# Optimization experiments

Hardware: AMD Instinct MI355X
Metric: run time of the kernel (lower is better)

Reference implementation:

```python
import jax, jax.numpy as jnp
import numpy as np
import math

DIM = 1024
HEADS = 16
B, N = 2, 2048

POLY = jnp.array([-0.037, 0.481, -2.3, 4.917, -1.791], dtype=jnp.float32)


def adaptive_temperature_softmax(logits):
    # logits: [b, h, n, n]
    original_probs = jax.nn.softmax(logits, axis=-1)
    entropy = jnp.sum(-original_probs * jnp.log(original_probs + 1e-9), axis=-1, keepdims=True)
    e2 = entropy * entropy
    poly_result = POLY[0] * e2 * e2 + POLY[1] * e2 * entropy + POLY[2] * e2 + POLY[3] * entropy + POLY[4]
    beta = jnp.where(entropy > 0.5, jnp.maximum(poly_result, 1.0), 1.0)
    return jax.nn.softmax(logits * beta, axis=-1)


def setup_inputs() -> dict:
    key = jax.random.key(0)
    ks = jax.random.split(key, 5)
    s = 1.0 / math.sqrt(DIM)
    return {
        "x": jax.random.normal(ks[0], (B, N, DIM), dtype=jnp.float32),
        "Wq": jax.random.normal(ks[1], (DIM, DIM), dtype=jnp.float32) * s,
        "Wk": jax.random.normal(ks[2], (DIM, DIM), dtype=jnp.float32) * s,
        "Wv": jax.random.normal(ks[3], (DIM, DIM), dtype=jnp.float32) * s,
        "Wo": jax.random.normal(ks[4], (DIM, DIM), dtype=jnp.float32) * s,
        "bo": jnp.zeros((DIM,), dtype=jnp.float32),
    }


def reference(x, Wq, Wk, Wv, Wo, bo):
    b, n, d = x.shape
    h = HEADS
    hd = d // h
    # torch nn.Linear: y = x @ W.T (+ bias)
    def proj(W):
        t = x @ W.T  # [b, n, d]
        return t.reshape(b, n, h, hd).transpose(0, 2, 1, 3)  # [b, h, n, hd]
    q, k, v = proj(Wq), proj(Wk), proj(Wv)
    sim = jnp.einsum('bhid,bhjd->bhij', q, k) / math.sqrt(hd)
    neg = -jnp.finfo(sim.dtype).max
    causal = jnp.triu(jnp.ones((n, n), dtype=bool), k=1)  # True above diagonal
    sim = jnp.where(causal, neg, sim)
    attn = adaptive_temperature_softmax(sim)
    out = jnp.einsum('bhij,bhjd->bhid', attn, v)
    out = out.transpose(0, 2, 1, 3).reshape(b, n, d)
    return out @ Wo.T + bo
```

## Files before the change

### kernel.cpp

```cpp
#include <hip/hip_runtime.h>
#include <math.h>

#define B_   2
#define N_   2048
#define D_   1024
#define H_   16
#define HD_  64
#define BH_  32
#define M_   4096

typedef __bf16 bf16x8 __attribute__((ext_vector_type(8)));
typedef float  f32x4  __attribute__((ext_vector_type(4)));

#define AS1_ __attribute__((address_space(1)))
#define AS3_ __attribute__((address_space(3)))
#define GLDS16(g, l) __builtin_amdgcn_global_load_lds( \
    (const AS1_ void*)(g), (AS3_ void*)(l), 16, 0, 0)

__device__ inline unsigned short f2b(float f) {
    unsigned u = __float_as_uint(f);
    u += 0x7FFFu + ((u >> 16) & 1u);
    return (unsigned short)(u >> 16);
}
__device__ inline unsigned short f2b_fast(float f) {
    return (unsigned short)((__float_as_uint(f) + 0x8000u) >> 16);
}

__global__ __launch_bounds__(256)
void cvt_all(const float* __restrict__ x,  const float* __restrict__ wq,
             const float* __restrict__ wk, const float* __restrict__ wv,
             const float* __restrict__ wo, ushort* __restrict__ dst)
{
    int i = blockIdx.x * 256 + threadIdx.x;
    if (i >= 2097152) return;
    int fi = i * 4;
    const float* s; int off;
    if (fi < 4194304) { s = x; off = fi; }
    else {
        int r = fi - 4194304;
        int wsel = r >> 20;
        off = r & 1048575;
        s = (wsel == 0) ? wq : (wsel == 1) ? wk : (wsel == 2) ? wv : wo;
    }
    float4 f = *(const float4*)(s + off);
    ushort4 o;
    o.x = f2b(f.x); o.y = f2b(f.y); o.z = f2b(f.z); o.w = f2b(f.w);
    *(ushort4*)(dst + fi) = o;
}

__global__ __launch_bounds__(256)
void gemm_qkv(const ushort* __restrict__ A,
              const ushort* __restrict__ W0, const ushort* __restrict__ W1,
              const ushort* __restrict__ W2,
              ushort* __restrict__ O0, ushort* __restrict__ O1,
              ushort* __restrict__ O2)
{
    const int z = blockIdx.z;
    const ushort* W = (z == 0) ? W0 : (z == 1) ? W1 : W2;

    __shared__ alignas(16) ushort As[128][32];
    __shared__ alignas(16) ushort Bs[128][32];

    const int t = threadIdx.x;
    const int lane = t & 63, w = t >> 6;
    const int quad = lane >> 4, l15 = lane & 15;
    const int wm = (w >> 1) * 64, wn = (w & 1) * 64;
    const int tileM = blockIdx.x * 128, tileN = blockIdx.y * 128;

    const int srow = lane >> 2, scol = (lane & 3) * 8;
    const ushort* GA = A + (size_t)(tileM + w * 16 + srow) * D_ + scol;
    const ushort* GB = W + (size_t)(tileN + w * 16 + srow) * D_ + scol;

    f32x4 acc[4][4];
#pragma unroll
    for (int mt = 0; mt < 4; ++mt)
#pragma unroll
        for (int nt = 0; nt < 4; ++nt) acc[mt][nt] = (f32x4){0.f, 0.f, 0.f, 0.f};

    for (int k0 = 0; k0 < D_; k0 += 32) {
        __syncthreads();
        GLDS16(GA + k0,            &As[w * 16][0]);
        GLDS16(GA + 64 * D_ + k0,  &As[64 + w * 16][0]);
        GLDS16(GB + k0,            &Bs[w * 16][0]);
        GLDS16(GB + 64 * D_ + k0,  &Bs[64 + w * 16][0]);
        __syncthreads();

        bf16x8 af[4], bf[4];
#pragma unroll
        for (int mt = 0; mt < 4; ++mt) af[mt] = *(const bf16x8*)&As[wm + mt * 16 + l15][quad * 8];
#pragma unroll
        for (int nt = 0; nt < 4; ++nt) bf[nt] = *(const bf16x8*)&Bs[wn + nt * 16 + l15][quad * 8];
#pragma unroll
        for (int mt = 0; mt < 4; ++mt)
#pragma unroll
            for (int nt = 0; nt < 4; ++nt)
                acc[mt][nt] = __builtin_amdgcn_mfma_f32_16x16x32_bf16(af[mt], bf[nt], acc[mt][nt], 0, 0, 0);
    }

    ushort* O = (z == 0) ? O0 : (z == 1) ? O1 : O2;
    const float scl = (z == 0) ? 0.18033688f : 1.0f;
#pragma unroll
    for (int mt = 0; mt < 4; ++mt)
#pragma unroll
        for (int nt = 0; nt < 4; ++nt) {
            if (z == 2) {
                int rg0 = tileM + wm + mt * 16 + quad * 4;
                int cgc = tileN + wn + nt * 16 + l15;
                int b = rg0 >> 11, n0 = rg0 & (N_ - 1);
                int h = cgc >> 6, dd = cgc & 63;
                ushort4 o4;
                o4.x = f2b(acc[mt][nt][0]); o4.y = f2b(acc[mt][nt][1]);
                o4.z = f2b(acc[mt][nt][2]); o4.w = f2b(acc[mt][nt][3]);
                *(ushort4*)&O[((size_t)((b * H_ + h) * HD_ + dd)) * N_ + n0] = o4;
            } else {
#pragma unroll
                for (int r = 0; r < 4; ++r) {
                    int rg = tileM + wm + mt * 16 + quad * 4 + r;
                    int cgc = tileN + wn + nt * 16 + l15;
                    int b = rg >> 11, n = rg & (N_ - 1);
                    int h = cgc >> 6, dd = cgc & 63;
                    O[(((size_t)(b * H_ + h)) * N_ + n) * HD_ + dd] = f2b(acc[mt][nt][r] * scl);
                }
            }
        }
}

__global__ __launch_bounds__(256)
void gemm_fin(const ushort* __restrict__ A, const ushort* __restrict__ W,
              const float* __restrict__ bias, float* __restrict__ Of)
{
    __shared__ alignas(16) ushort As[128][32];
    __shared__ alignas(16) ushort Bs[64][32];

    const int t = threadIdx.x;
    const int lane = t & 63, w = t >> 6;
    const int quad = lane >> 4, l15 = lane & 15;
    const int wm = (w >> 1) * 64, wn = (w & 1) * 32;
    const int tileM = blockIdx.x * 128, tileN = blockIdx.y * 64;

    const int srow = lane >> 2, scol = (lane & 3) * 8;
    const ushort* GA = A + (size_t)(tileM + w * 16 + srow) * D_ + scol;
    const ushort* GB = W + (size_t)(tileN + w * 16 + srow) * D_ + scol;

    f32x4 acc[4][2];
#pragma unroll
    for (int mt = 0; mt < 4; ++mt)
#pragma unroll
        for (int nt = 0; nt < 2; ++nt) acc[mt][nt] = (f32x4){0.f, 0.f, 0.f, 0.f};

    for (int k0 = 0; k0 < D_; k0 += 32) {
        __syncthreads();
        GLDS16(GA + k0,           &As[w * 16][0]);
        GLDS16(GA + 64 * D_ + k0, &As[64 + w * 16][0]);
        GLDS16(GB + k0,           &Bs[w * 16][0]);
        __syncthreads();

        bf16x8 af[4], bf[2];
#pragma unroll
        for (int mt = 0; mt < 4; ++mt) af[mt] = *(const bf16x8*)&As[wm + mt * 16 + l15][quad * 8];
#pragma unroll
        for (int nt = 0; nt < 2; ++nt) bf[nt] = *(const bf16x8*)&Bs[wn + nt * 16 + l15][quad * 8];
#pragma unroll
        for (int mt = 0; mt < 4; ++mt)
#pragma unroll
            for (int nt = 0; nt < 2; ++nt)
                acc[mt][nt] = __builtin_amdgcn_mfma_f32_16x16x32_bf16(af[mt], bf[nt], acc[mt][nt], 0, 0, 0);
    }

#pragma unroll
    for (int mt = 0; mt < 4; ++mt)
#pragma unroll
        for (int nt = 0; nt < 2; ++nt)
#pragma unroll
            for (int r = 0; r < 4; ++r) {
                int rg = tileM + wm + mt * 16 + quad * 4 + r;
                int cgc = tileN + wn + nt * 16 + l15;
                Of[(size_t)rg * D_ + cgc] = acc[mt][nt][r] + bias[cgc];
            }
}

__global__ __launch_bounds__(256)
void attn_mfma(const ushort* __restrict__ Q, const ushort* __restrict__ K,
               const ushort* __restrict__ VT, ushort* __restrict__ AO)
{
    const int bid = blockIdx.x;
    const int qt = 31 - (bid >> 5);
    const int bh = bid & 31;
    const size_t kvbase = (size_t)bh * N_ * HD_;

    __shared__ alignas(16) ushort Ks[128][72];
    __shared__ alignas(16) ushort Vs[64][136];
    __shared__ alignas(16) ushort Ps[4][4][296];

    const int t = threadIdx.x;
    const int lane = t & 63, w = t >> 6;
    const int quad = lane >> 4, l15 = lane & 15;
    const float SH2 = 11.5416913f;
    const float LN2 = 0.69314718f;

    const int skey = t >> 3;
    const int skc  = (t & 7) * 8;
    const ushort* KS = K + kvbase + (size_t)skey * HD_ + skc;
    const int vhd = t >> 4;
    const int vkc = (t & 15) * 8;
    const ushort* VS = VT + kvbase + (size_t)vhd * N_ + vkc;

    const int qrow = w * 16 + quad * 4;
    const int qglob = qt * 64 + qrow;
    const int b = bh >> 4, h = bh & 15;
    const int nCh = (qt + 2) >> 1;

    bf16x8 aq0, aq1;
    {
        const size_t qr = kvbase + (size_t)(qt * 64 + w * 16 + l15) * HD_;
        aq0 = *(const bf16x8*)&Q[qr + quad * 8];
        aq1 = *(const bf16x8*)&Q[qr + 32 + quad * 8];
    }

    float ez[4] = {0.f, 0.f, 0.f, 0.f};
    float sz[4] = {0.f, 0.f, 0.f, 0.f};

    uint4 k0 = *(const uint4*)KS;
    uint4 k1 = *(const uint4*)(KS + 32 * HD_);
    uint4 k2 = *(const uint4*)(KS + 64 * HD_);
    uint4 k3 = *(const uint4*)(KS + 96 * HD_);
    for (int c = 0; c < nCh; ++c) {
        __syncthreads();
        *(uint4*)&Ks[skey][skc]      = k0;
        *(uint4*)&Ks[32 + skey][skc] = k1;
        *(uint4*)&Ks[64 + skey][skc] = k2;
        *(uint4*)&Ks[96 + skey][skc] = k3;
        __syncthreads();
        if (c + 1 < nCh) {
            const ushort* nb = KS + (size_t)(c + 1) * (128 * HD_);
            k0 = *(const uint4*)nb;
            k1 = *(const uint4*)(nb + 32 * HD_);
            k2 = *(const uint4*)(nb + 64 * HD_);
            k3 = *(const uint4*)(nb + 96 * HD_);
        }
        if (c + 1 < nCh) {
#pragma unroll
            for (int nt = 0; nt < 8; ++nt) {
                f32x4 sv = (f32x4){-SH2, -SH2, -SH2, -SH2};
                sv = __builtin_amdgcn_mfma_f32_16x16x32_bf16(aq0, *(const bf16x8*)&Ks[nt * 16 + l15][quad * 8], sv, 0, 0, 0);
                sv = __builtin_amdgcn_mfma_f32_16x16x32_bf16(aq1, *(const bf16x8*)&Ks[nt * 16 + l15][32 + quad * 8], sv, 0, 0, 0);
#pragma unroll
                for (int r = 0; r < 4; ++r) {
                    float sh = sv[r];
                    float e = __builtin_amdgcn_exp2f(sh);
                    ez[r] += e;
                    sz[r] = fmaf(e, sh, sz[r]);
                }
            }
        } else {
            const int tiles = (((qt + 1) * 64) - c * 128) >> 4;
            const int kb0 = c * 128;
            for (int nt = 0; nt < tiles; ++nt) {
                f32x4 sv = (f32x4){-SH2, -SH2, -SH2, -SH2};
                sv = __builtin_amdgcn_mfma_f32_16x16x32_bf16(aq0, *(const bf16x8*)&Ks[nt * 16 + l15][quad * 8], sv, 0, 0, 0);
                sv = __builtin_amdgcn_mfma_f32_16x16x32_bf16(aq1, *(const bf16x8*)&Ks[nt * 16 + l15][32 + quad * 8], sv, 0, 0, 0);
                const int kcol = kb0 + nt * 16 + l15;
#pragma unroll
                for (int r = 0; r < 4; ++r) {
                    float sh = sv[r];
                    float e = (kcol <= qglob + r) ? __builtin_amdgcn_exp2f(sh) : 0.f;
                    ez[r] += e;
                    sz[r] = fmaf(e, sh, sz[r]);
                }
            }
        }
    }
#pragma unroll
    for (int r = 0; r < 4; ++r) {
#pragma unroll
        for (int off = 1; off < 16; off <<= 1) {
            ez[r] += __shfl_xor(ez[r], off);
            sz[r] += __shfl_xor(sz[r], off);
        }
    }

    float bl[4];
#pragma unroll
    for (int r = 0; r < 4; ++r) {
        float Z = ez[r];
        float Hh = LN2 * (__builtin_amdgcn_logf(Z) - sz[r] / Z);
        float bb = 1.f;
        if (Hh > 0.5f) {
            float e2 = Hh * Hh;
            float pp = -0.037f * e2 * e2 + 0.481f * e2 * Hh - 2.3f * e2 + 4.917f * Hh - 1.791f;
            bb = fmaxf(pp, 1.f);
        }
        bl[r] = bb;
    }

    f32x4 ov[4];
#pragma unroll
    for (int nt = 0; nt < 4; ++nt) ov[nt] = (f32x4){0.f, 0.f, 0.f, 0.f};
    float zp[4] = {0.f, 0.f, 0.f, 0.f};

    k0 = *(const uint4*)KS;
    k1 = *(const uint4*)(KS + 32 * HD_);
    k2 = *(const uint4*)(KS + 64 * HD_);
    k3 = *(const uint4*)(KS + 96 * HD_);
    uint4 v0 = *(const uint4*)VS;
    uint4 v1 = *(const uint4*)(VS + 16 * N_);
    uint4 v2 = *(const uint4*)(VS + 32 * N_);
    uint4 v3 = *(const uint4*)(VS + 48 * N_);
    for (int c = 0; c < nCh; ++c) {
        __syncthreads();
        *(uint4*)&Ks[skey][skc]      = k0;
        *(uint4*)&Ks[32 + skey][skc] = k1;
        *(uint4*)&Ks[64 + skey][skc] = k2;
        *(uint4*)&Ks[96 + skey][skc] = k3;
        *(uint4*)&Vs[vhd][vkc]       = v0;
        *(uint4*)&Vs[16 + vhd][vkc]  = v1;
        *(uint4*)&Vs[32 + vhd][vkc]  = v2;
        *(uint4*)&Vs[48 + vhd][vkc]  = v3;
        __syncthreads();
        if (c + 1 < nCh) {
            const ushort* nk = KS + (size_t)(c + 1) * (128 * HD_);
            k0 = *(const uint4*)nk;
            k1 = *(const uint4*)(nk + 32 * HD_);
            k2 = *(const uint4*)(nk + 64 * HD_);
            k3 = *(const uint4*)(nk + 96 * HD_);
            const ushort* nv = VS + (c + 1) * 128;
            v0 = *(const uint4*)nv;
            v1 = *(const uint4*)(nv + 16 * N_);
            v2 = *(const uint4*)(nv + 32 * N_);
            v3 = *(const uint4*)(nv + 48 * N_);
        }
        const int halves = min(2, (qt + 1) - c * 2);
        for (int hh = 0; hh < halves; ++hh) {
            const bool diag = (c * 2 + hh == qt);

            float wv[4][4];
#pragma unroll
            for (int nt = 0; nt < 4; ++nt) {
                f32x4 sv = (f32x4){-SH2, -SH2, -SH2, -SH2};
                sv = __builtin_amdgcn_mfma_f32_16x16x32_bf16(aq0, *(const bf16x8*)&Ks[hh * 64 + nt * 16 + l15][quad * 8], sv, 0, 0, 0);
                sv = __builtin_amdgcn_mfma_f32_16x16x32_bf16(aq1, *(const bf16x8*)&Ks[hh * 64 + nt * 16 + l15][32 + quad * 8], sv, 0, 0, 0);
                const int kcol = nt * 16 + l15;
#pragma unroll
                for (int r = 0; r < 4; ++r) {
                    float e = __builtin_amdgcn_exp2f(bl[r] * sv[r]);
                    wv[nt][r] = (!diag || (kcol <= qrow + r)) ? e : 0.f;
                }
            }
#pragma unroll
            for (int nt = 0; nt < 4; ++nt)
#pragma unroll
                for (int r = 0; r < 4; ++r)
                    Ps[w][quad][r * 72 + nt * 16 + l15] = f2b_fast(wv[nt][r]);
#pragma unroll
            for (int r = 0; r < 4; ++r)
                zp[r] += (wv[0][r] + wv[1][r]) + (wv[2][r] + wv[3][r]);

            bf16x8 pa0 = *(const bf16x8*)&Ps[w][l15 >> 2][(l15 & 3) * 72 + quad * 8];
            bf16x8 pa1 = *(const bf16x8*)&Ps[w][l15 >> 2][(l15 & 3) * 72 + 32 + quad * 8];
#pragma unroll
            for (int nt = 0; nt < 4; ++nt) {
                ov[nt] = __builtin_amdgcn_mfma_f32_16x16x32_bf16(pa0, *(const bf16x8*)&Vs[nt * 16 + l15][hh * 64 + quad * 8], ov[nt], 0, 0, 0);
                ov[nt] = __builtin_amdgcn_mfma_f32_16x16x32_bf16(pa1, *(const bf16x8*)&Vs[nt * 16 + l15][hh * 64 + 32 + quad * 8], ov[nt], 0, 0, 0);
            }
        }
    }
#pragma unroll
    for (int r = 0; r < 4; ++r)
#pragma unroll
        for (int off = 1; off < 16; off <<= 1) zp[r] += __shfl_xor(zp[r], off);

#pragma unroll
    for (int r = 0; r < 4; ++r) {
        int qg = qt * 64 + w * 16 + quad * 4 + r;
        float inv = 1.f / zp[r];
        size_t rowoff = ((size_t)(b * N_ + qg)) * D_ + h * HD_;
#pragma unroll
        for (int nt = 0; nt < 4; ++nt)
            AO[rowoff + nt * 16 + l15] = f2b(ov[nt][r] * inv);
    }
}

extern "C" void kernel_launch(void* const* d_in, const int* in_sizes, int n_in,
                              void* d_out, int out_size, void* d_ws, size_t ws_size,
                              hipStream_t stream)
{
    const float* x  = (const float*)d_in[0];
    const float* Wq = (const float*)d_in[1];
    const float* Wk = (const float*)d_in[2];
    const float* Wv = (const float*)d_in[3];
    const float* Wo = (const float*)d_in[4];
    const float* bo = (const float*)d_in[5];
    float* out = (float*)d_out;

    ushort* ws  = (ushort*)d_ws;
    ushort* xb  = ws;
    ushort* wqb = ws + 4194304;
    ushort* wkb = ws + 5242880;
    ushort* wvb = ws + 6291456;
    ushort* wob = ws + 7340032;
    ushort* Qb  = ws + 8388608;
    ushort* Kb  = ws + 12582912;
    ushort* Vtb = ws + 16777216;
    ushort* aob = ws + 20971520;

    cvt_all<<<8192, 256, 0, stream>>>(x, Wq, Wk, Wv, Wo, xb);

    gemm_qkv<<<dim3(32, 8, 3), 256, 0, stream>>>(
        xb, wqb, wkb, wvb, Qb, Kb, Vtb);

    attn_mfma<<<dim3(1024), 256, 0, stream>>>(Qb, Kb, Vtb, aob);

    gemm_fin<<<dim3(32, 16), 256, 0, stream>>>(aob, wob, bo, out);
}
```

Before: 207.7 us.

## Double-buffer LDS tiles in QKV and output projection GEMMs

Both projection GEMMs now use two shared-memory buffers. The next K-slice is issued with global_load_lds while MFMAs run on the current slice, and only one barrier is used per iteration instead of two. The aim is to hide global load latency behind compute, at the cost of doubled LDS use per block, which could lower occupancy. The sync before reuse relies on the barrier also waiting for the async LDS loads to land.

After: 202.7 us. -2.4%, faster.

```diff
diff --git a/kernel.cpp b/kernel.cpp
--- a/kernel.cpp
+++ b/kernel.cpp
@@ -58,8 +58,8 @@
     const int z = blockIdx.z;
     const ushort* W = (z == 0) ? W0 : (z == 1) ? W1 : W2;
 
-    __shared__ alignas(16) ushort As[128][32];
-    __shared__ alignas(16) ushort Bs[128][32];
+    __shared__ alignas(16) ushort As[2][128][32];
+    __shared__ alignas(16) ushort Bs[2][128][32];
 
     const int t = threadIdx.x;
     const int lane = t & 63, w = t >> 6;
@@ -67,9 +67,8 @@
     const int wm = (w >> 1) * 64, wn = (w & 1) * 64;
     const int tileM = blockIdx.x * 128, tileN = blockIdx.y * 128;
 
-    const int srow = lane >> 2, scol = (lane & 3) * 8;
-    const ushort* GA = A + (size_t)(tileM + w * 16 + srow) * D_ + scol;
-    const ushort* GB = W + (size_t)(tileN + w * 16 + srow) * D_ + scol;
+    const ushort* GA = A + (size_t)(tileM + w * 16 + (lane >> 2)) * D_ + (lane & 3) * 8;
+    const ushort* GB = W + (size_t)(tileN + w * 16 + (lane >> 2)) * D_ + (lane & 3) * 8;
 
     f32x4 acc[4][4];
 #pragma unroll
@@ -77,24 +76,35 @@
 #pragma unroll
         for (int nt = 0; nt < 4; ++nt) acc[mt][nt] = (f32x4){0.f, 0.f, 0.f, 0.f};
 
+    GLDS16(GA,            &As[0][w * 16][0]);
+    GLDS16(GA + 64 * D_,  &As[0][64 + w * 16][0]);
+    GLDS16(GB,            &Bs[0][w * 16][0]);
+    GLDS16(GB + 64 * D_,  &Bs[0][64 + w * 16][0]);
+    __syncthreads();
+
+    int cur = 0;
     for (int k0 = 0; k0 < D_; k0 += 32) {
-        __syncthreads();
-        GLDS16(GA + k0,            &As[w * 16][0]);
-        GLDS16(GA + 64 * D_ + k0,  &As[64 + w * 16][0]);
-        GLDS16(GB + k0,            &Bs[w * 16][0]);
-        GLDS16(GB + 64 * D_ + k0,  &Bs[64 + w * 16][0]);
-        __syncthreads();
+        const int nxt = cur ^ 1;
+        if (k0 + 32 < D_) {
+            GLDS16(GA + k0 + 32,           &As[nxt][w * 16][0]);
+            GLDS16(GA + 64 * D_ + k0 + 32, &As[nxt][64 + w * 16][0]);
+            GLDS16(GB + k0 + 32,           &Bs[nxt][w * 16][0]);
+            GLDS16(GB + 64 * D_ + k0 + 32, &Bs[nxt][64 + w * 16][0]);
+        }
 
         bf16x8 af[4], bf[4];
 #pragma unroll
-        for (int mt = 0; mt < 4; ++mt) af[mt] = *(const bf16x8*)&As[wm + mt * 16 + l15][quad * 8];
-#pragma unroll
-        for (int nt = 0; nt < 4; ++nt) bf[nt] = *(const bf16x8*)&Bs[wn + nt * 16 + l15][quad * 8];
+        for (int mt = 0; mt < 4; ++mt) af[mt] = *(const bf16x8*)&As[cur][wm + mt * 16 + l15][quad * 8];
+#pragma unroll
+        for (int nt = 0; nt < 4; ++nt) bf[nt] = *(const bf16x8*)&Bs[cur][wn + nt * 16 + l15][quad * 8];
 #pragma unroll
         for (int mt = 0; mt < 4; ++mt)
 #pragma unroll
             for (int nt = 0; nt < 4; ++nt)
                 acc[mt][nt] = __builtin_amdgcn_mfma_f32_16x16x32_bf16(af[mt], bf[nt], acc[mt][nt], 0, 0, 0);
+
+        __syncthreads();
+        cur = nxt;
     }
 
     ushort* O = (z == 0) ? O0 : (z == 1) ? O1 : O2;
@@ -129,8 +139,8 @@
 void gemm_fin(const ushort* __restrict__ A, const ushort* __restrict__ W,
               const float* __restrict__ bias, float* __restrict__ Of)
 {
-    __shared__ alignas(16) ushort As[128][32];
-    __shared__ alignas(16) ushort Bs[64][32];
+    __shared__ alignas(16) ushort As[2][128][32];
+    __shared__ alignas(16) ushort Bs[2][64][32];
 
     const int t = threadIdx.x;
     const int lane = t & 63, w = t >> 6;
@@ -138,9 +148,8 @@
     const int wm = (w >> 1) * 64, wn = (w & 1) * 32;
     const int tileM = blockIdx.x * 128, tileN = blockIdx.y * 64;
 
-    const int srow = lane >> 2, scol = (lane & 3) * 8;
-    const ushort* GA = A + (size_t)(tileM + w * 16 + srow) * D_ + scol;
-    const ushort* GB = W + (size_t)(tileN + w * 16 + srow) * D_ + scol;
+    const ushort* GA = A + (size_t)(tileM + w * 16 + (lane >> 2)) * D_ + (lane & 3) * 8;
+    const ushort* GB = W + (size_t)(tileN + w * 16 + (lane >> 2)) * D_ + (lane & 3) * 8;
 
     f32x4 acc[4][2];
 #pragma unroll
@@ -148,23 +157,33 @@
 #pragma unroll
         for (int nt = 0; nt < 2; ++nt) acc[mt][nt] = (f32x4){0.f, 0.f, 0.f, 0.f};
 
+    GLDS16(GA,           &As[0][w * 16][0]);
+    GLDS16(GA + 64 * D_, &As[0][64 + w * 16][0]);
+    GLDS16(GB,           &Bs[0][w * 16][0]);
+    __syncthreads();
+
+    int cur = 0;
     for (int k0 = 0; k0 < D_; k0 += 32) {
-        __syncthreads();
-        GLDS16(GA + k0,           &As[w * 16][0]);
-        GLDS16(GA + 64 * D_ + k0, &As[64 + w * 16][0]);
-        GLDS16(GB + k0,           &Bs[w * 16][0]);
-        __syncthreads();
+        const int nxt = cur ^ 1;
+        if (k0 + 32 < D_) {
+            GLDS16(GA + k0 + 32,           &As[nxt][w * 16][0]);
+            GLDS16(GA + 64 * D_ + k0 + 32, &As[nxt][64 + w * 16][0]);
+            GLDS16(GB + k0 + 32,           &Bs[nxt][w * 16][0]);
+        }
 
         bf16x8 af[4], bf[2];
 #pragma unroll
-        for (int mt = 0; mt < 4; ++mt) af[mt] = *(const bf16x8*)&As[wm + mt * 16 + l15][quad * 8];
-#pragma unroll
-        for (int nt = 0; nt < 2; ++nt) bf[nt] = *(const bf16x8*)&Bs[wn + nt * 16 + l15][quad * 8];
+        for (int mt = 0; mt < 4; ++mt) af[mt] = *(const bf16x8*)&As[cur][wm + mt * 16 + l15][quad * 8];
+#pragma unroll
+        for (int nt = 0; nt < 2; ++nt) bf[nt] = *(const bf16x8*)&Bs[cur][wn + nt * 16 + l15][quad * 8];
 #pragma unroll
         for (int mt = 0; mt < 4; ++mt)
 #pragma unroll
             for (int nt = 0; nt < 2; ++nt)
                 acc[mt][nt] = __builtin_amdgcn_mfma_f32_16x16x32_bf16(af[mt], bf[nt], acc[mt][nt], 0, 0, 0);
+
+        __syncthreads();
+        cur = nxt;
     }
 
 #pragma unroll
```
